# Performance work log

Hardware: AMD Instinct MI355X
Metric: run time of the kernel (lower is better)

Reference implementation:

```python
import jax, jax.numpy as jnp
import numpy as np

N_NODES = 10000
N_EDGES = 160000
NEG_SLOPE = 0.2


def _gat_layer(x, src, dst, W, a_src, a_dst, bias, concat):
    # x: [N, F_in]; W: [F_in, H*C]; a_src/a_dst: [H, C]; bias: [H*C] or [C]
    N = x.shape[0]
    H, C = a_src.shape
    h = (x @ W).reshape(N, H, C)                       # [N,H,C]
    al_s = jnp.einsum('nhc,hc->nh', h, a_src)          # [N,H]
    al_d = jnp.einsum('nhc,hc->nh', h, a_dst)          # [N,H]
    e = jax.nn.leaky_relu(al_s[src] + al_d[dst], NEG_SLOPE)  # [E,H]
    # segment softmax over incoming edges of each destination node
    m = jax.ops.segment_max(e, dst, num_segments=N)    # [N,H]
    ex = jnp.exp(e - m[dst])
    denom = jax.ops.segment_sum(ex, dst, num_segments=N)
    alpha = ex / (denom[dst] + 1e-16)                  # [E,H]
    msg = h[src] * alpha[:, :, None]                   # [E,H,C]
    out = jax.ops.segment_sum(msg, dst, num_segments=N)  # [N,H,C]
    out = out.reshape(N, H * C) if concat else out.mean(axis=1)
    return out + bias


def setup_inputs() -> dict:
    key = jax.random.key(0)
    ks = jax.random.split(key, 10)
    in_dim, hid, out_dim, heads = 768, 512, 768, 4
    x = jax.random.normal(ks[0], (N_NODES, in_dim), dtype=jnp.float32)
    edge_index = jax.random.randint(ks[1], (2, N_EDGES), 0, N_NODES, dtype=jnp.int64)
    g = lambda k, shape, fan: jax.random.normal(k, shape, jnp.float32) / np.sqrt(fan)
    return {
        'x': x,
        'edge_index': edge_index,
        'W1': g(ks[2], (in_dim, heads * hid), in_dim),
        'att_src1': g(ks[3], (heads, hid), hid),
        'att_dst1': g(ks[4], (heads, hid), hid),
        'b1': jnp.zeros((heads * hid,), jnp.float32),
        'W2': g(ks[5], (heads * hid, out_dim), heads * hid),
        'att_src2': g(ks[6], (1, out_dim), out_dim),
        'att_dst2': g(ks[7], (1, out_dim), out_dim),
        'b2': jnp.zeros((out_dim,), jnp.float32),
    }


def reference(x, edge_index, W1, att_src1, att_dst1, b1, W2, att_src2, att_dst2, b2):
    N = x.shape[0]
    loops = jnp.arange(N, dtype=edge_index.dtype)
    src = jnp.concatenate([edge_index[0], loops])  # PyG GATConv adds self-loops
    dst = jnp.concatenate([edge_index[1], loops])
    h = jax.nn.elu(_gat_layer(x, src, dst, W1, att_src1, att_dst1, b1, concat=True))
    out = _gat_layer(h, src, dst, W2, att_src2, att_dst2, b2, concat=False)
    return out
```

## Files before the change

### kernel.cpp

```cpp
#include <hip/hip_runtime.h>
#include <hip/hip_bf16.h>
#include <math.h>

#define N_NODES 10000
#define N_EDGES0 160000
#define E_TOT (N_EDGES0 + N_NODES)
#define H1 4
#define C1 512
#define F1 2048
#define IN_DIM 768
#define C2 768
#define NEG_SLOPE 0.2f

typedef _Float16 f16x8 __attribute__((ext_vector_type(8)));
typedef _Float16 f16x4 __attribute__((ext_vector_type(4)));
typedef float f32x4 __attribute__((ext_vector_type(4)));

typedef __attribute__((address_space(1))) const void* gas_ptr;
typedef __attribute__((address_space(3))) void* las_ptr;
static __device__ __forceinline__ void gload16(const void* g, void* l) {
  __builtin_amdgcn_global_load_lds((gas_ptr)g, (las_ptr)l, 16, 0, 0);
}

static __device__ __forceinline__ unsigned enc_f(float v) {
  unsigned u = __float_as_uint(v);
  return (u & 0x80000000u) ? ~u : (u | 0x80000000u);
}
static __device__ __forceinline__ float dec_f(unsigned u) {
  return (u & 0x80000000u) ? __uint_as_float(u ^ 0x80000000u)
                           : __uint_as_float(~u);
}

static __device__ __forceinline__ void edge_sd(const int* __restrict__ ei, int e,
                                               int& s, int& d) {
  if (e < N_EDGES0) { s = ei[e]; d = ei[N_EDGES0 + e]; }
  else { s = e - N_EDGES0; d = s; }
}

__global__ void split_k(const float* __restrict__ in, _Float16* __restrict__ hi,
                        _Float16* __restrict__ lo, int n4) {
  int i = blockIdx.x * blockDim.x + threadIdx.x;
  if (i >= n4) return;
  float4 v = ((const float4*)in)[i];
  f16x4 h, l;
  h.x = (_Float16)v.x; l.x = (_Float16)(v.x - (float)h.x);
  h.y = (_Float16)v.y; l.y = (_Float16)(v.y - (float)h.y);
  h.z = (_Float16)v.z; l.z = (_Float16)(v.z - (float)h.z);
  h.w = (_Float16)v.w; l.w = (_Float16)(v.w - (float)h.w);
  ((f16x4*)hi)[i] = h;
  ((f16x4*)lo)[i] = l;
}

__global__ void tsplit_k(const float* __restrict__ W, _Float16* __restrict__ hi,
                         _Float16* __restrict__ lo, int K, int N) {
  __shared__ float tile[32][33];
  const int nb = blockIdx.x * 32, kb = blockIdx.y * 32;
  const int tx = threadIdx.x, ty = threadIdx.y;
  for (int r = ty; r < 32; r += 8)
    tile[r][tx] = W[(size_t)(kb + r) * N + nb + tx];
  __syncthreads();
  for (int r = ty; r < 32; r += 8) {
    float v = tile[tx][r];
    _Float16 h = (_Float16)v;
    hi[(size_t)(nb + r) * K + kb + tx] = h;
    lo[(size_t)(nb + r) * K + kb + tx] = (_Float16)(v - (float)h);
  }
}

__global__ __launch_bounds__(256) void gemm_sf16(
    const _Float16* __restrict__ Ahi, const _Float16* __restrict__ Alo,
    const _Float16* __restrict__ Bhi, const _Float16* __restrict__ Blo,
    float* __restrict__ C, int M, int N, int K,
    const float* __restrict__ asrc, const float* __restrict__ adst,
    float* __restrict__ als, float* __restrict__ ald, int Hh, int Cdim) {
  __shared__ _Float16 sAh[128 * 32];
  __shared__ _Float16 sAl[128 * 32];
  __shared__ _Float16 sBh[128 * 32];
  __shared__ _Float16 sBl[128 * 32];

  const int t = threadIdx.x;
  const int w = t >> 6, lane = t & 63;
  const int m0 = blockIdx.y * 128, n0 = blockIdx.x * 128;

  const int o0 = w * 1024 + lane * 16;
  const int o1 = o0 + 4096;
  const int ma0 = o0 >> 6, cb0 = o0 & 63;
  const int ma1 = o1 >> 6, cb1 = o1 & 63;
  const int rA0 = min(m0 + ma0, M - 1), rA1 = min(m0 + ma1, M - 1);
  const size_t gA0 = (size_t)rA0 * K + (cb0 >> 1);
  const size_t gA1 = (size_t)rA1 * K + (cb1 >> 1);
  const size_t gB0 = (size_t)(n0 + ma0) * K + (cb0 >> 1);
  const size_t gB1 = (size_t)(n0 + ma1) * K + (cb1 >> 1);

  char* lA0 = (char*)sAh + w * 1024;
  char* lA1 = lA0 + 4096;
  char* lAl0 = (char*)sAl + w * 1024;
  char* lAl1 = lAl0 + 4096;
  char* lB0 = (char*)sBh + w * 1024;
  char* lB1 = lB0 + 4096;
  char* lBl0 = (char*)sBl + w * 1024;
  char* lBl1 = lBl0 + 4096;

  const int wr = w >> 1, wc = w & 1;
  const int lr = lane & 15, lg = lane >> 4;
  const int aoff = (wr * 64 + lr) * 32 + lg * 8;
  const int boff = (wc * 64 + lr) * 32 + lg * 8;

  f32x4 acc[4][4];
#pragma unroll
  for (int i = 0; i < 4; i++)
#pragma unroll
    for (int j = 0; j < 4; j++) acc[i][j] = (f32x4)(0.f);

  for (int k0 = 0; k0 < K; k0 += 32) {
    __syncthreads();
    gload16(Ahi + gA0 + k0, lA0);
    gload16(Ahi + gA1 + k0, lA1);
    gload16(Alo + gA0 + k0, lAl0);
    gload16(Alo + gA1 + k0, lAl1);
    gload16(Bhi + gB0 + k0, lB0);
    gload16(Bhi + gB1 + k0, lB1);
    gload16(Blo + gB0 + k0, lBl0);
    gload16(Blo + gB1 + k0, lBl1);
    __syncthreads();

    f16x8 ah[4], al[4], bh[4], bl[4];
#pragma unroll
    for (int i = 0; i < 4; i++) {
      ah[i] = *(const f16x8*)&sAh[aoff + i * 16 * 32];
      al[i] = *(const f16x8*)&sAl[aoff + i * 16 * 32];
      bh[i] = *(const f16x8*)&sBh[boff + i * 16 * 32];
      bl[i] = *(const f16x8*)&sBl[boff + i * 16 * 32];
    }
#pragma unroll
    for (int i = 0; i < 4; i++)
#pragma unroll
      for (int j = 0; j < 4; j++) {
        acc[i][j] = __builtin_amdgcn_mfma_f32_16x16x32_f16(ah[i], bh[j], acc[i][j], 0, 0, 0);
        acc[i][j] = __builtin_amdgcn_mfma_f32_16x16x32_f16(ah[i], bl[j], acc[i][j], 0, 0, 0);
        acc[i][j] = __builtin_amdgcn_mfma_f32_16x16x32_f16(al[i], bh[j], acc[i][j], 0, 0, 0);
      }
  }

#pragma unroll
  for (int i = 0; i < 4; i++)
#pragma unroll
    for (int j = 0; j < 4; j++) {
      const int col = n0 + wc * 64 + j * 16 + lr;
      const int rbase = m0 + wr * 64 + i * 16 + lg * 4;
#pragma unroll
      for (int r = 0; r < 4; r++) {
        int row = rbase + r;
        if (row < M) C[(size_t)row * N + col] = acc[i][j][r];
      }
    }

  const int head = n0 / Cdim;
  const int cbase = n0 - head * Cdim + wc * 64 + lr;
  float asv[4], adv[4];
#pragma unroll
  for (int j = 0; j < 4; j++) {
    asv[j] = asrc[(size_t)head * Cdim + cbase + j * 16];
    adv[j] = adst[(size_t)head * Cdim + cbase + j * 16];
  }
#pragma unroll
  for (int i = 0; i < 4; i++) {
    const int rbase = m0 + wr * 64 + i * 16 + lg * 4;
#pragma unroll
    for (int r = 0; r < 4; r++) {
      float ss = 0.f, sd = 0.f;
#pragma unroll
      for (int j = 0; j < 4; j++) {
        float v = acc[i][j][r];
        ss = fmaf(v, asv[j], ss);
        sd = fmaf(v, adv[j], sd);
      }
#pragma unroll
      for (int o = 8; o; o >>= 1) {
        ss += __shfl_xor(ss, o);
        sd += __shfl_xor(sd, o);
      }
      if (lr == 0 && rbase + r < M) {
        atomicAdd(&als[(size_t)(rbase + r) * Hh + head], ss);
        atomicAdd(&ald[(size_t)(rbase + r) * Hh + head], sd);
      }
    }
  }
}

__global__ void edge_max_k(const int* __restrict__ ei,
                           const float* __restrict__ als,
                           const float* __restrict__ ald,
                           float* __restrict__ ev, unsigned* __restrict__ menc,
                           int Hh) {
  int idx = blockIdx.x * blockDim.x + threadIdx.x;
  if (idx >= E_TOT * Hh) return;
  int e = idx / Hh, hh = idx - e * Hh;
  int s, d; edge_sd(ei, e, s, d);
  float x = als[s * Hh + hh] + ald[d * Hh + hh];
  float v = x > 0.f ? x : NEG_SLOPE * x;
  ev[idx] = v;
  atomicMax(&menc[d * Hh + hh], enc_f(v));
}

__global__ void edge_exp_k(const int* __restrict__ ei,
                           const unsigned* __restrict__ menc,
                           const float* __restrict__ ev,
                           const int* __restrict__ csr_pos,
                           float* __restrict__ evs, float* __restrict__ denom,
                           int Hh) {
  int idx = blockIdx.x * blockDim.x + threadIdx.x;
  if (idx >= E_TOT * Hh) return;
  int e = idx / Hh, hh = idx - e * Hh;
  int s, d; edge_sd(ei, e, s, d);
  float m = dec_f(menc[d * Hh + hh]);
  float ex = expf(ev[idx] - m);
  evs[(size_t)csr_pos[e] * Hh + hh] = ex;
  atomicAdd(&denom[d * Hh + hh], ex);
}

__global__ void hist_k(const int* __restrict__ ei, int* __restrict__ count) {
  int e = blockIdx.x * blockDim.x + threadIdx.x;
  if (e >= E_TOT) return;
  int s, d; edge_sd(ei, e, s, d);
  atomicAdd(&count[d], 1);
}

__global__ __launch_bounds__(1024) void scan_k(const int* __restrict__ count,
                                               int* __restrict__ rowstart,
                                               int N, int total) {
  __shared__ int sums[1024];
  __shared__ int carry_s;
  int t = threadIdx.x;
  if (t == 0) carry_s = 0;
  __syncthreads();
  for (int base = 0; base < N; base += 1024) {
    int i = base + t;
    int c = (i < N) ? count[i] : 0;
    sums[t] = c;
    __syncthreads();
    for (int off = 1; off < 1024; off <<= 1) {
      int v = (t >= off) ? sums[t - off] : 0;
      __syncthreads();
      sums[t] += v;
      __syncthreads();
    }
    int carry = carry_s;
    if (i < N) rowstart[i] = carry + sums[t] - c;
    __syncthreads();
    if (t == 1023) carry_s = carry + sums[1023];
    __syncthreads();
  }
  if (t == 0) rowstart[N] = total;
}

__global__ void scatter_k(const int* __restrict__ ei,
                          const int* __restrict__ rowstart,
                          int* __restrict__ cursor,
                          int* __restrict__ csr_src, int* __restrict__ csr_pos) {
  int e = blockIdx.x * blockDim.x + threadIdx.x;
  if (e >= E_TOT) return;
  int s, d; edge_sd(ei, e, s, d);
  int pos = rowstart[d] + atomicAdd(&cursor[d], 1);
  csr_src[pos] = s;
  csr_pos[e] = pos;
}

template <int FT, bool ELU, bool SPLIT>
__global__ __launch_bounds__(256) void aggregate_k(
    const float* __restrict__ hsrc, const float* __restrict__ evs,
    const float* __restrict__ denom, const float* __restrict__ bias,
    const int* __restrict__ rowstart, const int* __restrict__ csr_src,
    float* __restrict__ out,
    _Float16* __restrict__ ohi, _Float16* __restrict__ olo,
    int Hh, int C) {
  const int n = blockIdx.x;
  const int t = threadIdx.x;
  const int F = Hh * C;
  const int f0 = t * FT;
  const int hh = f0 / C;
  const float inv = 1.f / (denom[n * Hh + hh] + 1e-16f);
  float acc[FT];
#pragma unroll
  for (int i = 0; i < FT; i++) acc[i] = 0.f;
  const int j0 = rowstart[n], j1 = rowstart[n + 1];

  constexpr int UN = (FT == 8) ? 4 : 8;
  int j = j0;
  for (; j + UN <= j1; j += UN) {
    int   sidx[UN];
    float wv[UN];
#pragma unroll
    for (int u = 0; u < UN; u++) sidx[u] = csr_src[j + u];
#pragma unroll
    for (int u = 0; u < UN; u++) wv[u] = evs[(size_t)(j + u) * Hh + hh];
    float4 va[UN][FT / 4];
#pragma unroll
    for (int u = 0; u < UN; u++) {
      const float* hp = hsrc + (size_t)sidx[u] * F + f0;
#pragma unroll
      for (int q = 0; q < FT / 4; q++) va[u][q] = *(const float4*)(hp + q * 4);
    }
#pragma unroll
    for (int u = 0; u < UN; u++)
#pragma unroll
      for (int q = 0; q < FT / 4; q++) {
        acc[q * 4 + 0] = fmaf(wv[u], va[u][q].x, acc[q * 4 + 0]);
        acc[q * 4 + 1] = fmaf(wv[u], va[u][q].y, acc[q * 4 + 1]);
        acc[q * 4 + 2] = fmaf(wv[u], va[u][q].z, acc[q * 4 + 2]);
        acc[q * 4 + 3] = fmaf(wv[u], va[u][q].w, acc[q * 4 + 3]);
      }
  }
  for (; j < j1; j++) {
    int s = csr_src[j];
    float wgt = evs[(size_t)j * Hh + hh];
    const float* hp = hsrc + (size_t)s * F + f0;
#pragma unroll
    for (int q = 0; q < FT / 4; q++) {
      float4 v = *(const float4*)(hp + q * 4);
      acc[q * 4 + 0] = fmaf(wgt, v.x, acc[q * 4 + 0]);
      acc[q * 4 + 1] = fmaf(wgt, v.y, acc[q * 4 + 1]);
      acc[q * 4 + 2] = fmaf(wgt, v.z, acc[q * 4 + 2]);
      acc[q * 4 + 3] = fmaf(wgt, v.w, acc[q * 4 + 3]);
    }
  }

  if (SPLIT) {
    f16x8 h, l;
#pragma unroll
    for (int i = 0; i < FT; i++) {
      float o = acc[i] * inv + bias[f0 + i];
      if (ELU) o = o > 0.f ? o : expm1f(o);
      _Float16 hv = (_Float16)o;
      h[i & 7] = hv;
      l[i & 7] = (_Float16)(o - (float)hv);
    }
    *(f16x8*)&ohi[(size_t)n * F + f0] = h;
    *(f16x8*)&olo[(size_t)n * F + f0] = l;
  } else {
#pragma unroll
    for (int i = 0; i < FT; i++) {
      float o = acc[i] * inv + bias[f0 + i];
      if (ELU) o = o > 0.f ? o : expm1f(o);
      out[(size_t)n * F + f0 + i] = o;
    }
  }
}

extern "C" void kernel_launch(void* const* d_in, const int* in_sizes, int n_in,
                              void* d_out, int out_size, void* d_ws, size_t ws_size,
                              hipStream_t stream) {
  const float* x   = (const float*)d_in[0];
  const int*   ei  = (const int*)d_in[1];
  const float* W1  = (const float*)d_in[2];
  const float* as1 = (const float*)d_in[3];
  const float* ad1 = (const float*)d_in[4];
  const float* b1  = (const float*)d_in[5];
  const float* W2  = (const float*)d_in[6];
  const float* as2 = (const float*)d_in[7];
  const float* ad2 = (const float*)d_in[8];
  const float* b2  = (const float*)d_in[9];
  float* out = (float*)d_out;

  char* p = (char*)d_ws;
  auto alloc = [&](size_t bytes) {
    char* r = p;
    p += (bytes + 255) & ~(size_t)255;
    return r;
  };
  float*     h1    = (float*)alloc((size_t)N_NODES * F1 * 4);
  _Float16*  xhi   = (_Float16*)alloc((size_t)N_NODES * IN_DIM * 2);
  _Float16*  xlo   = (_Float16*)alloc((size_t)N_NODES * IN_DIM * 2);
  _Float16*  W1hi  = (_Float16*)alloc((size_t)IN_DIM * F1 * 2);
  _Float16*  W1lo  = (_Float16*)alloc((size_t)IN_DIM * F1 * 2);
  _Float16*  W2hi  = (_Float16*)alloc((size_t)F1 * C2 * 2);
  _Float16*  W2lo  = (_Float16*)alloc((size_t)F1 * C2 * 2);
  _Float16*  h2hi  = (_Float16*)alloc((size_t)N_NODES * F1 * 2);
  _Float16*  h2lo  = (_Float16*)alloc((size_t)N_NODES * F1 * 2);
  float*     als   = (float*)alloc((size_t)N_NODES * H1 * 4);
  float*     ald   = (float*)alloc((size_t)N_NODES * H1 * 4);
  unsigned*  menc  = (unsigned*)alloc((size_t)N_NODES * H1 * 4);
  float*     denom = (float*)alloc((size_t)N_NODES * H1 * 4);
  float*     ev    = (float*)alloc((size_t)E_TOT * H1 * 4);
  float*     evs   = (float*)alloc((size_t)E_TOT * H1 * 4);
  int*       count    = (int*)alloc((size_t)N_NODES * 4);
  int*       rowstart = (int*)alloc((size_t)(N_NODES + 1) * 4);
  int*       cursor   = (int*)alloc((size_t)N_NODES * 4);
  int*       csr_src  = (int*)alloc((size_t)E_TOT * 4);
  int*       csr_pos  = (int*)alloc((size_t)E_TOT * 4);
  float*     h3 = h1;

  const int EB = (E_TOT + 255) / 256;

  hipMemsetAsync(count, 0, (size_t)N_NODES * 4, stream);
  hipMemsetAsync(cursor, 0, (size_t)N_NODES * 4, stream);
  hist_k<<<EB, 256, 0, stream>>>(ei, count);
  scan_k<<<1, 1024, 0, stream>>>(count, rowstart, N_NODES, E_TOT);
  scatter_k<<<EB, 256, 0, stream>>>(ei, rowstart, cursor, csr_src, csr_pos);

  split_k<<<(N_NODES * IN_DIM / 4 + 255) / 256, 256, 0, stream>>>(x, xhi, xlo,
                                                                  N_NODES * IN_DIM / 4);
  tsplit_k<<<dim3(F1 / 32, IN_DIM / 32), dim3(32, 8), 0, stream>>>(W1, W1hi, W1lo,
                                                                   IN_DIM, F1);
  tsplit_k<<<dim3(C2 / 32, F1 / 32), dim3(32, 8), 0, stream>>>(W2, W2hi, W2lo,
                                                               F1, C2);

  hipMemsetAsync(als, 0, (size_t)N_NODES * H1 * 4, stream);
  hipMemsetAsync(ald, 0, (size_t)N_NODES * H1 * 4, stream);
  gemm_sf16<<<dim3(F1 / 128, (N_NODES + 127) / 128), 256, 0, stream>>>(
      xhi, xlo, W1hi, W1lo, h1, N_NODES, F1, IN_DIM,
      as1, ad1, als, ald, H1, C1);
  hipMemsetAsync(menc, 0, (size_t)N_NODES * H1 * 4, stream);
  hipMemsetAsync(denom, 0, (size_t)N_NODES * H1 * 4, stream);
  edge_max_k<<<(E_TOT * H1 + 255) / 256, 256, 0, stream>>>(ei, als, ald, ev, menc, H1);
  edge_exp_k<<<(E_TOT * H1 + 255) / 256, 256, 0, stream>>>(ei, menc, ev, csr_pos,
                                                           evs, denom, H1);
  aggregate_k<8, true, true><<<N_NODES, 256, 0, stream>>>(
      h1, evs, denom, b1, rowstart, csr_src, nullptr, h2hi, h2lo, H1, C1);

  hipMemsetAsync(als, 0, (size_t)N_NODES * 4, stream);
  hipMemsetAsync(ald, 0, (size_t)N_NODES * 4, stream);
  gemm_sf16<<<dim3(C2 / 128, (N_NODES + 127) / 128), 256, 0, stream>>>(
      h2hi, h2lo, W2hi, W2lo, h3, N_NODES, C2, F1,
      as2, ad2, als, ald, 1, C2);
  hipMemsetAsync(menc, 0, (size_t)N_NODES * 4, stream);
  hipMemsetAsync(denom, 0, (size_t)N_NODES * 4, stream);
  edge_max_k<<<EB, 256, 0, stream>>>(ei, als, ald, ev, menc, 1);
  edge_exp_k<<<EB, 256, 0, stream>>>(ei, menc, ev, csr_pos, evs, denom, 1);
  aggregate_k<4, false, false><<<N_NODES, 192, 0, stream>>>(
      h3, evs, denom, b2, rowstart, csr_src, out, nullptr, nullptr, 1, C2);
}
```

Baseline: 737.6 us.

## Reorder layer-1 GAT: aggregate raw features before projection, precompute attention logits

Layer 1 now computes the attention logits directly from x by first folding the attention vectors into W1 (W1·a per head). It then aggregates the 768-wide input features per head with the softmax weights, and only after that runs the projection GEMM, with bias, ELU and the hi/lo split fused into the GEMM epilogue. This avoids aggregating the 2048-wide fp32 h1 and drops the separate x split kernel. The cost is a 4x-wider GEMM A operand (per-head aggregated x, 3072 columns of which each output block reads its own head's slice) and an extra intermediate of N×3072 fp16 hi/lo.

```diff
diff --git a/kernel.cpp b/kernel.cpp
--- a/kernel.cpp
+++ b/kernel.cpp
@@ -35,20 +35,6 @@
                                                int& s, int& d) {
   if (e < N_EDGES0) { s = ei[e]; d = ei[N_EDGES0 + e]; }
   else { s = e - N_EDGES0; d = s; }
-}
-
-__global__ void split_k(const float* __restrict__ in, _Float16* __restrict__ hi,
-                        _Float16* __restrict__ lo, int n4) {
-  int i = blockIdx.x * blockDim.x + threadIdx.x;
-  if (i >= n4) return;
-  float4 v = ((const float4*)in)[i];
-  f16x4 h, l;
-  h.x = (_Float16)v.x; l.x = (_Float16)(v.x - (float)h.x);
-  h.y = (_Float16)v.y; l.y = (_Float16)(v.y - (float)h.y);
-  h.z = (_Float16)v.z; l.z = (_Float16)(v.z - (float)h.z);
-  h.w = (_Float16)v.w; l.w = (_Float16)(v.w - (float)h.w);
-  ((f16x4*)hi)[i] = h;
-  ((f16x4*)lo)[i] = l;
 }
 
 __global__ void tsplit_k(const float* __restrict__ W, _Float16* __restrict__ hi,
@@ -67,10 +53,64 @@
   }
 }
 
+__global__ void proj_attn_k(const float* __restrict__ W1,
+                            const float* __restrict__ as1,
+                            const float* __restrict__ ad1,
+                            float* __restrict__ ws, float* __restrict__ wd) {
+  int wv = (blockIdx.x * blockDim.x + threadIdx.x) >> 6;
+  int lane = threadIdx.x & 63;
+  if (wv >= H1 * IN_DIM) return;
+  int h = wv / IN_DIM, k = wv - h * IN_DIM;
+  const float* wrow = W1 + (size_t)k * F1 + h * C1;
+  const float* sa = as1 + h * C1;
+  const float* da = ad1 + h * C1;
+  float ss = 0.f, sd = 0.f;
+  for (int c = lane; c < C1; c += 64) {
+    float v = wrow[c];
+    ss = fmaf(v, sa[c], ss);
+    sd = fmaf(v, da[c], sd);
+  }
+#pragma unroll
+  for (int o = 32; o; o >>= 1) { ss += __shfl_xor(ss, o); sd += __shfl_xor(sd, o); }
+  if (lane == 0) { ws[(size_t)h * IN_DIM + k] = ss; wd[(size_t)h * IN_DIM + k] = sd; }
+}
+
+__global__ void logits1_k(const float* __restrict__ x,
+                          const float* __restrict__ ws, const float* __restrict__ wd,
+                          float* __restrict__ als, float* __restrict__ ald) {
+  int n = (blockIdx.x * blockDim.x + threadIdx.x) >> 6;
+  int lane = threadIdx.x & 63;
+  if (n >= N_NODES) return;
+  const float* xp = x + (size_t)n * IN_DIM;
+  float ss[H1] = {0.f, 0.f, 0.f, 0.f}, sd[H1] = {0.f, 0.f, 0.f, 0.f};
+  for (int k = lane; k < IN_DIM; k += 64) {
+    float xv = xp[k];
+#pragma unroll
+    for (int h = 0; h < H1; h++) {
+      ss[h] = fmaf(xv, ws[h * IN_DIM + k], ss[h]);
+      sd[h] = fmaf(xv, wd[h * IN_DIM + k], sd[h]);
+    }
+  }
+#pragma unroll
+  for (int h = 0; h < H1; h++)
+#pragma unroll
+    for (int o = 32; o; o >>= 1) { ss[h] += __shfl_xor(ss[h], o); sd[h] += __shfl_xor(sd[h], o); }
+  if (lane == 0) {
+#pragma unroll
+    for (int h = 0; h < H1; h++) {
+      als[(size_t)n * H1 + h] = ss[h];
+      ald[(size_t)n * H1 + h] = sd[h];
+    }
+  }
+}
+
+template <bool SPLITOUT>
 __global__ __launch_bounds__(256) void gemm_sf16(
     const _Float16* __restrict__ Ahi, const _Float16* __restrict__ Alo,
     const _Float16* __restrict__ Bhi, const _Float16* __restrict__ Blo,
-    float* __restrict__ C, int M, int N, int K,
+    int M, int N, int K, int lda, int nch,
+    float* __restrict__ C, const float* __restrict__ bias,
+    _Float16* __restrict__ ohi, _Float16* __restrict__ olo,
     const float* __restrict__ asrc, const float* __restrict__ adst,
     float* __restrict__ als, float* __restrict__ ald, int Hh, int Cdim) {
   __shared__ _Float16 sAh[128 * 32];
@@ -81,14 +121,15 @@
   const int t = threadIdx.x;
   const int w = t >> 6, lane = t & 63;
   const int m0 = blockIdx.y * 128, n0 = blockIdx.x * 128;
+  const size_t hofs = (size_t)(n0 / nch) * K;
 
   const int o0 = w * 1024 + lane * 16;
   const int o1 = o0 + 4096;
   const int ma0 = o0 >> 6, cb0 = o0 & 63;
   const int ma1 = o1 >> 6, cb1 = o1 & 63;
   const int rA0 = min(m0 + ma0, M - 1), rA1 = min(m0 + ma1, M - 1);
-  const size_t gA0 = (size_t)rA0 * K + (cb0 >> 1);
-  const size_t gA1 = (size_t)rA1 * K + (cb1 >> 1);
+  const size_t gA0 = (size_t)rA0 * lda + hofs + (cb0 >> 1);
+  const size_t gA1 = (size_t)rA1 * lda + hofs + (cb1 >> 1);
   const size_t gB0 = (size_t)(n0 + ma0) * K + (cb0 >> 1);
   const size_t gB1 = (size_t)(n0 + ma1) * K + (cb1 >> 1);
 
@@ -142,47 +183,70 @@
       }
   }
 
-#pragma unroll
-  for (int i = 0; i < 4; i++)
+  if constexpr (SPLITOUT) {
 #pragma unroll
     for (int j = 0; j < 4; j++) {
       const int col = n0 + wc * 64 + j * 16 + lr;
+      const float bv = bias[col];
+#pragma unroll
+      for (int i = 0; i < 4; i++) {
+        const int rbase = m0 + wr * 64 + i * 16 + lg * 4;
+#pragma unroll
+        for (int r = 0; r < 4; r++) {
+          const int row = rbase + r;
+          if (row < M) {
+            float o = acc[i][j][r] + bv;
+            o = o > 0.f ? o : expm1f(o);
+            _Float16 hv = (_Float16)o;
+            ohi[(size_t)row * N + col] = hv;
+            olo[(size_t)row * N + col] = (_Float16)(o - (float)hv);
+          }
+        }
+      }
+    }
+  } else {
+#pragma unroll
+    for (int i = 0; i < 4; i++)
+#pragma unroll
+      for (int j = 0; j < 4; j++) {
+        const int col = n0 + wc * 64 + j * 16 + lr;
+        const int rbase = m0 + wr * 64 + i * 16 + lg * 4;
+#pragma unroll
+        for (int r = 0; r < 4; r++) {
+          int row = rbase + r;
+          if (row < M) C[(size_t)row * N + col] = acc[i][j][r];
+        }
+      }
+
+    const int head = n0 / Cdim;
+    const int cbase = n0 - head * Cdim + wc * 64 + lr;
+    float asv[4], adv[4];
+#pragma unroll
+    for (int j = 0; j < 4; j++) {
+      asv[j] = asrc[(size_t)head * Cdim + cbase + j * 16];
+      adv[j] = adst[(size_t)head * Cdim + cbase + j * 16];
+    }
+#pragma unroll
+    for (int i = 0; i < 4; i++) {
       const int rbase = m0 + wr * 64 + i * 16 + lg * 4;
 #pragma unroll
       for (int r = 0; r < 4; r++) {
-        int row = rbase + r;
-        if (row < M) C[(size_t)row * N + col] = acc[i][j][r];
-      }
-    }
-
-  const int head = n0 / Cdim;
-  const int cbase = n0 - head * Cdim + wc * 64 + lr;
-  float asv[4], adv[4];
-#pragma unroll
-  for (int j = 0; j < 4; j++) {
-    asv[j] = asrc[(size_t)head * Cdim + cbase + j * 16];
-    adv[j] = adst[(size_t)head * Cdim + cbase + j * 16];
-  }
-#pragma unroll
-  for (int i = 0; i < 4; i++) {
-    const int rbase = m0 + wr * 64 + i * 16 + lg * 4;
-#pragma unroll
-    for (int r = 0; r < 4; r++) {
-      float ss = 0.f, sd = 0.f;
-#pragma unroll
-      for (int j = 0; j < 4; j++) {
-        float v = acc[i][j][r];
-        ss = fmaf(v, asv[j], ss);
-        sd = fmaf(v, adv[j], sd);
-      }
-#pragma unroll
-      for (int o = 8; o; o >>= 1) {
-        ss += __shfl_xor(ss, o);
-        sd += __shfl_xor(sd, o);
-      }
-      if (lr == 0 && rbase + r < M) {
-        atomicAdd(&als[(size_t)(rbase + r) * Hh + head], ss);
-        atomicAdd(&ald[(size_t)(rbase + r) * Hh + head], sd);
+        float ss = 0.f, sd = 0.f;
+#pragma unroll
+        for (int j = 0; j < 4; j++) {
+          float v = acc[i][j][r];
+          ss = fmaf(v, asv[j], ss);
+          sd = fmaf(v, adv[j], sd);
+        }
+#pragma unroll
+        for (int o = 8; o; o >>= 1) {
+          ss += __shfl_xor(ss, o);
+          sd += __shfl_xor(sd, o);
+        }
+        if (lr == 0 && rbase + r < M) {
+          atomicAdd(&als[(size_t)(rbase + r) * Hh + head], ss);
+          atomicAdd(&ald[(size_t)(rbase + r) * Hh + head], sd);
+        }
       }
     }
   }
@@ -266,14 +330,81 @@
   csr_pos[e] = pos;
 }
 
-template <int FT, bool ELU, bool SPLIT>
+__global__ __launch_bounds__(192) void aggregate_x_k(
+    const float* __restrict__ x, const float* __restrict__ evs,
+    const float* __restrict__ denom, const int* __restrict__ rowstart,
+    const int* __restrict__ csr_src,
+    _Float16* __restrict__ ohi, _Float16* __restrict__ olo) {
+  const int n = blockIdx.x;
+  const int f0 = threadIdx.x * 4;
+  float inv[H1];
+#pragma unroll
+  for (int h = 0; h < H1; h++) inv[h] = 1.f / (denom[n * H1 + h] + 1e-16f);
+  float acc[H1][4];
+#pragma unroll
+  for (int h = 0; h < H1; h++)
+#pragma unroll
+    for (int q = 0; q < 4; q++) acc[h][q] = 0.f;
+
+  const int j0 = rowstart[n], j1 = rowstart[n + 1];
+  int j = j0;
+  for (; j + 4 <= j1; j += 4) {
+    int sidx[4];
+    float4 wv[4], xv[4];
+#pragma unroll
+    for (int u = 0; u < 4; u++) sidx[u] = csr_src[j + u];
+#pragma unroll
+    for (int u = 0; u < 4; u++) wv[u] = *(const float4*)&evs[(size_t)(j + u) * H1];
+#pragma unroll
+    for (int u = 0; u < 4; u++)
+      xv[u] = *(const float4*)(x + (size_t)sidx[u] * IN_DIM + f0);
+#pragma unroll
+    for (int u = 0; u < 4; u++) {
+      const float* pw = (const float*)&wv[u];
+#pragma unroll
+      for (int h = 0; h < H1; h++) {
+        acc[h][0] = fmaf(pw[h], xv[u].x, acc[h][0]);
+        acc[h][1] = fmaf(pw[h], xv[u].y, acc[h][1]);
+        acc[h][2] = fmaf(pw[h], xv[u].z, acc[h][2]);
+        acc[h][3] = fmaf(pw[h], xv[u].w, acc[h][3]);
+      }
+    }
+  }
+  for (; j < j1; j++) {
+    int s = csr_src[j];
+    float4 wv = *(const float4*)&evs[(size_t)j * H1];
+    float4 xv = *(const float4*)(x + (size_t)s * IN_DIM + f0);
+    const float* pw = (const float*)&wv;
+#pragma unroll
+    for (int h = 0; h < H1; h++) {
+      acc[h][0] = fmaf(pw[h], xv.x, acc[h][0]);
+      acc[h][1] = fmaf(pw[h], xv.y, acc[h][1]);
+      acc[h][2] = fmaf(pw[h], xv.z, acc[h][2]);
+      acc[h][3] = fmaf(pw[h], xv.w, acc[h][3]);
+    }
+  }
+
+#pragma unroll
+  for (int h = 0; h < H1; h++) {
+    f16x4 h4, l4;
+#pragma unroll
+    for (int q = 0; q < 4; q++) {
+      float o = acc[h][q] * inv[h];
+      _Float16 hv = (_Float16)o;
+      h4[q] = hv;
+      l4[q] = (_Float16)(o - (float)hv);
+    }
+    *(f16x4*)&ohi[(size_t)n * (H1 * IN_DIM) + h * IN_DIM + f0] = h4;
+    *(f16x4*)&olo[(size_t)n * (H1 * IN_DIM) + h * IN_DIM + f0] = l4;
+  }
+}
+
+template <int FT>
 __global__ __launch_bounds__(256) void aggregate_k(
     const float* __restrict__ hsrc, const float* __restrict__ evs,
     const float* __restrict__ denom, const float* __restrict__ bias,
     const int* __restrict__ rowstart, const int* __restrict__ csr_src,
-    float* __restrict__ out,
-    _Float16* __restrict__ ohi, _Float16* __restrict__ olo,
-    int Hh, int C) {
+    float* __restrict__ out, int Hh, int C) {
   const int n = blockIdx.x;
   const int t = threadIdx.x;
   const int F = Hh * C;
@@ -285,7 +416,7 @@
   for (int i = 0; i < FT; i++) acc[i] = 0.f;
   const int j0 = rowstart[n], j1 = rowstart[n + 1];
 
-  constexpr int UN = (FT == 8) ? 4 : 8;
+  constexpr int UN = 8;
   int j = j0;
   for (; j + UN <= j1; j += UN) {
     int   sidx[UN];
@@ -324,27 +455,9 @@
       acc[q * 4 + 3] = fmaf(wgt, v.w, acc[q * 4 + 3]);
     }
   }
-
-  if (SPLIT) {
-    f16x8 h, l;
-#pragma unroll
-    for (int i = 0; i < FT; i++) {
-      float o = acc[i] * inv + bias[f0 + i];
-      if (ELU) o = o > 0.f ? o : expm1f(o);
-      _Float16 hv = (_Float16)o;
-      h[i & 7] = hv;
-      l[i & 7] = (_Float16)(o - (float)hv);
-    }
-    *(f16x8*)&ohi[(size_t)n * F + f0] = h;
-    *(f16x8*)&olo[(size_t)n * F + f0] = l;
-  } else {
-#pragma unroll
-    for (int i = 0; i < FT; i++) {
-      float o = acc[i] * inv + bias[f0 + i];
-      if (ELU) o = o > 0.f ? o : expm1f(o);
-      out[(size_t)n * F + f0 + i] = o;
-    }
-  }
+#pragma unroll
+  for (int i = 0; i < FT; i++)
+    out[(size_t)n * F + f0 + i] = acc[i] * inv + bias[f0 + i];
 }
 
 extern "C" void kernel_launch(void* const* d_in, const int* in_sizes, int n_in,
@@ -368,27 +481,28 @@
     p += (bytes + 255) & ~(size_t)255;
     return r;
   };
-  float*     h1    = (float*)alloc((size_t)N_NODES * F1 * 4);
-  _Float16*  xhi   = (_Float16*)alloc((size_t)N_NODES * IN_DIM * 2);
-  _Float16*  xlo   = (_Float16*)alloc((size_t)N_NODES * IN_DIM * 2);
-  _Float16*  W1hi  = (_Float16*)alloc((size_t)IN_DIM * F1 * 2);
-  _Float16*  W1lo  = (_Float16*)alloc((size_t)IN_DIM * F1 * 2);
-  _Float16*  W2hi  = (_Float16*)alloc((size_t)F1 * C2 * 2);
-  _Float16*  W2lo  = (_Float16*)alloc((size_t)F1 * C2 * 2);
-  _Float16*  h2hi  = (_Float16*)alloc((size_t)N_NODES * F1 * 2);
-  _Float16*  h2lo  = (_Float16*)alloc((size_t)N_NODES * F1 * 2);
-  float*     als   = (float*)alloc((size_t)N_NODES * H1 * 4);
-  float*     ald   = (float*)alloc((size_t)N_NODES * H1 * 4);
-  unsigned*  menc  = (unsigned*)alloc((size_t)N_NODES * H1 * 4);
-  float*     denom = (float*)alloc((size_t)N_NODES * H1 * 4);
-  float*     ev    = (float*)alloc((size_t)E_TOT * H1 * 4);
-  float*     evs   = (float*)alloc((size_t)E_TOT * H1 * 4);
-  int*       count    = (int*)alloc((size_t)N_NODES * 4);
-  int*       rowstart = (int*)alloc((size_t)(N_NODES + 1) * 4);
-  int*       cursor   = (int*)alloc((size_t)N_NODES * 4);
-  int*       csr_src  = (int*)alloc((size_t)E_TOT * 4);
-  int*       csr_pos  = (int*)alloc((size_t)E_TOT * 4);
-  float*     h3 = h1;
+  _Float16* xahi  = (_Float16*)alloc((size_t)N_NODES * H1 * IN_DIM * 2);
+  _Float16* xalo  = (_Float16*)alloc((size_t)N_NODES * H1 * IN_DIM * 2);
+  _Float16* W1hi  = (_Float16*)alloc((size_t)IN_DIM * F1 * 2);
+  _Float16* W1lo  = (_Float16*)alloc((size_t)IN_DIM * F1 * 2);
+  _Float16* W2hi  = (_Float16*)alloc((size_t)F1 * C2 * 2);
+  _Float16* W2lo  = (_Float16*)alloc((size_t)F1 * C2 * 2);
+  _Float16* h2hi  = (_Float16*)alloc((size_t)N_NODES * F1 * 2);
+  _Float16* h2lo  = (_Float16*)alloc((size_t)N_NODES * F1 * 2);
+  float*    ws1   = (float*)alloc((size_t)H1 * IN_DIM * 4);
+  float*    wd1   = (float*)alloc((size_t)H1 * IN_DIM * 4);
+  float*    als   = (float*)alloc((size_t)N_NODES * H1 * 4);
+  float*    ald   = (float*)alloc((size_t)N_NODES * H1 * 4);
+  unsigned* menc  = (unsigned*)alloc((size_t)N_NODES * H1 * 4);
+  float*    denom = (float*)alloc((size_t)N_NODES * H1 * 4);
+  float*    ev    = (float*)alloc((size_t)E_TOT * H1 * 4);
+  float*    evs   = (float*)alloc((size_t)E_TOT * H1 * 4);
+  int*      count    = (int*)alloc((size_t)N_NODES * 4);
+  int*      rowstart = (int*)alloc((size_t)(N_NODES + 1) * 4);
+  int*      cursor   = (int*)alloc((size_t)N_NODES * 4);
+  int*      csr_src  = (int*)alloc((size_t)E_TOT * 4);
+  int*      csr_pos  = (int*)alloc((size_t)E_TOT * 4);
+  float*    h3 = (float*)xahi;
 
   const int EB = (E_TOT + 255) / 256;
 
@@ -398,35 +512,33 @@
   scan_k<<<1, 1024, 0, stream>>>(count, rowstart, N_NODES, E_TOT);
   scatter_k<<<EB, 256, 0, stream>>>(ei, rowstart, cursor, csr_src, csr_pos);
 
-  split_k<<<(N_NODES * IN_DIM / 4 + 255) / 256, 256, 0, stream>>>(x, xhi, xlo,
-                                                                  N_NODES * IN_DIM / 4);
   tsplit_k<<<dim3(F1 / 32, IN_DIM / 32), dim3(32, 8), 0, stream>>>(W1, W1hi, W1lo,
                                                                    IN_DIM, F1);
   tsplit_k<<<dim3(C2 / 32, F1 / 32), dim3(32, 8), 0, stream>>>(W2, W2hi, W2lo,
                                                                F1, C2);
-
-  hipMemsetAsync(als, 0, (size_t)N_NODES * H1 * 4, stream);
-  hipMemsetAsync(ald, 0, (size_t)N_NODES * H1 * 4, stream);
-  gemm_sf16<<<dim3(F1 / 128, (N_NODES + 127) / 128), 256, 0, stream>>>(
-      xhi, xlo, W1hi, W1lo, h1, N_NODES, F1, IN_DIM,
-      as1, ad1, als, ald, H1, C1);
+  proj_attn_k<<<(H1 * IN_DIM * 64) / 256, 256, 0, stream>>>(W1, as1, ad1, ws1, wd1);
+
+  logits1_k<<<(N_NODES * 64 + 255) / 256, 256, 0, stream>>>(x, ws1, wd1, als, ald);
   hipMemsetAsync(menc, 0, (size_t)N_NODES * H1 * 4, stream);
   hipMemsetAsync(denom, 0, (size_t)N_NODES * H1 * 4, stream);
   edge_max_k<<<(E_TOT * H1 + 255) / 256, 256, 0, stream>>>(ei, als, ald, ev, menc, H1);
   edge_exp_k<<<(E_TOT * H1 + 255) / 256, 256, 0, stream>>>(ei, menc, ev, csr_pos,
                                                            evs, denom, H1);
-  aggregate_k<8, true, true><<<N_NODES, 256, 0, stream>>>(
-      h1, evs, denom, b1, rowstart, csr_src, nullptr, h2hi, h2lo, H1, C1);
+  aggregate_x_k<<<N_NODES, 192, 0, stream>>>(x, evs, denom, rowstart, csr_src,
+                                             xahi, xalo);
+  gemm_sf16<true><<<dim3(F1 / 128, (N_NODES + 127) / 128), 256, 0, stream>>>(
+      xahi, xalo, W1hi, W1lo, N_NODES, F1, IN_DIM, H1 * IN_DIM, C1,
+      nullptr, b1, h2hi, h2lo, nullptr, nullptr, nullptr, nullptr, 0, C1);
 
   hipMemsetAsync(als, 0, (size_t)N_NODES * 4, stream);
   hipMemsetAsync(ald, 0, (size_t)N_NODES * 4, stream);
-  gemm_sf16<<<dim3(C2 / 128, (N_NODES + 127) / 128), 256, 0, stream>>>(
-      h2hi, h2lo, W2hi, W2lo, h3, N_NODES, C2, F1,
-      as2, ad2, als, ald, 1, C2);
+  gemm_sf16<false><<<dim3(C2 / 128, (N_NODES + 127) / 128), 256, 0, stream>>>(
+      h2hi, h2lo, W2hi, W2lo, N_NODES, C2, F1, F1, 1 << 30,
+      h3, nullptr, nullptr, nullptr, as2, ad2, als, ald, 1, C2);
   hipMemsetAsync(menc, 0, (size_t)N_NODES * 4, stream);
   hipMemsetAsync(denom, 0, (size_t)N_NODES * 4, stream);
   edge_max_k<<<EB, 256, 0, stream>>>(ei, als, ald, ev, menc, 1);
   edge_exp_k<<<EB, 256, 0, stream>>>(ei, menc, ev, csr_pos, evs, denom, 1);
-  aggregate_k<4, false, false><<<N_NODES, 192, 0, stream>>>(
-      h3, evs, denom, b2, rowstart, csr_src, out, nullptr, nullptr, 1, C2);
-}
+  aggregate_k<4><<<N_NODES, 192, 0, stream>>>(h3, evs, denom, b2, rowstart,
+                                              csr_src, out, 1, C2);
+}
```

Result: faster. 640.6 us (-13.2%).
